# Kernel tuning notes

Hardware: AMD Instinct MI355X
Metric: run time of the kernel (lower is better)

The kernel has to match this reference:

```python
import jax, jax.numpy as jnp
import numpy as np

N, C, HID, B, K = 10000, 64, 64, 32, 2

def setup_inputs() -> dict:
    key = jax.random.key(0)
    k1, k2, k3, k4 = jax.random.split(key, 4)
    return {
        "x": jax.random.normal(k1, (B, N, C), dtype=jnp.float32),
        "node_embeddings": jax.random.normal(k2, (N, C, C), dtype=jnp.float32),
        "weights_pool": jax.random.normal(k3, (K, N, C, HID), dtype=jnp.float32),
        "bias_pool": jax.random.normal(k4, (N, HID), dtype=jnp.float32),
    }

def reference(x, node_embeddings, weights_pool, bias_pool):
    # supports: per-node adjacency-like mixing matrix, softmax(relu(.)) over last dim
    supports = jax.nn.softmax(jax.nn.relu(node_embeddings), axis=2)  # (n, c, c)
    # k=0 support is identity -> x_g[:,0] == x (no need to materialize eye)
    x_g1 = jnp.einsum('bnc,ncm->bnm', x, supports)                    # (b, n, c)
    # x_gconv = sum_k x_g[k] @ W[k] per node, + per-node bias
    out = (jnp.einsum('bnm,nmo->bno', x, weights_pool[0])
           + jnp.einsum('bnm,nmo->bno', x_g1, weights_pool[1])
           + bias_pool)                                               # (b, n, hid)
    return out
```

## Files before the change

### kernel.cpp

```cpp
#include <hip/hip_runtime.h>
#include <hip/hip_bf16.h>


constexpr int N_ = 10000;
constexpr int C_ = 64;
constexpr int H_ = 64;
constexpr int B_ = 32;
constexpr int STP = 67;

typedef __bf16 bf16x8 __attribute__((ext_vector_type(8)));
typedef float  f32x4  __attribute__((ext_vector_type(4)));

__global__ __launch_bounds__(256, 2) void avwgcn_kernel(
    const float* __restrict__ x,
    const float* __restrict__ emb,
    const float* __restrict__ wpool,
    const float* __restrict__ bias,
    float* __restrict__ out)
{
    __shared__ float st[64 * STP];
    __shared__ float g1[32 * STP];

    const int n = blockIdx.x;
    const int t = threadIdx.x;
    const int w = t >> 6;
    const int l = t & 63;
    const int r = l & 15;
    const int g = l >> 4;

    {
        const int c = t >> 2;
        const int q = t & 3;
        const float* ep = emb + (size_t)n * (C_ * C_) + c * C_ + q * 16;
        float v[16];
        #pragma unroll
        for (int i = 0; i < 4; ++i) {
            float4 e4 = *reinterpret_cast<const float4*>(ep + i * 4);
            v[i * 4 + 0] = e4.x; v[i * 4 + 1] = e4.y;
            v[i * 4 + 2] = e4.z; v[i * 4 + 3] = e4.w;
        }
        float s = 0.f;
        #pragma unroll
        for (int i = 0; i < 16; ++i) {
            float e = __expf(fmaxf(v[i], 0.f));
            v[i] = e;
            s += e;
        }
        s += __shfl_xor(s, 1);
        s += __shfl_xor(s, 2);
        const float inv = 1.0f / s;
        #pragma unroll
        for (int i = 0; i < 16; ++i)
            st[(q * 16 + i) * STP + c] = v[i] * inv;
    }

    bf16x8 xa[2][2];
    #pragma unroll
    for (int mt = 0; mt < 2; ++mt) {
        #pragma unroll
        for (int kt = 0; kt < 2; ++kt) {
            const float* xp = x + (size_t)(mt * 16 + r) * (N_ * C_)
                                + (size_t)n * C_ + kt * 32 + g * 8;
            float4 a0 = *reinterpret_cast<const float4*>(xp);
            float4 a1 = *reinterpret_cast<const float4*>(xp + 4);
            bf16x8 f;
            f[0] = (__bf16)a0.x; f[1] = (__bf16)a0.y;
            f[2] = (__bf16)a0.z; f[3] = (__bf16)a0.w;
            f[4] = (__bf16)a1.x; f[5] = (__bf16)a1.y;
            f[6] = (__bf16)a1.z; f[7] = (__bf16)a1.w;
            xa[mt][kt] = f;
        }
    }

    __syncthreads();

    f32x4 accg[2];
    accg[0] = (f32x4){0.f, 0.f, 0.f, 0.f};
    accg[1] = (f32x4){0.f, 0.f, 0.f, 0.f};
    #pragma unroll
    for (int kt = 0; kt < 2; ++kt) {
        const float* sp = st + (w * 16 + r) * STP + kt * 32 + g * 8;
        bf16x8 sb;
        #pragma unroll
        for (int i = 0; i < 8; ++i) sb[i] = (__bf16)sp[i];
        #pragma unroll
        for (int mt = 0; mt < 2; ++mt)
            accg[mt] = __builtin_amdgcn_mfma_f32_16x16x32_bf16(
                xa[mt][kt], sb, accg[mt], 0, 0, 0);
    }

    #pragma unroll
    for (int mt = 0; mt < 2; ++mt)
        #pragma unroll
        for (int ri = 0; ri < 4; ++ri)
            g1[(mt * 16 + g * 4 + ri) * STP + (w * 16 + r)] = accg[mt][ri];

    __syncthreads();

    bf16x8 ga[2][2];
    #pragma unroll
    for (int mt = 0; mt < 2; ++mt) {
        #pragma unroll
        for (int kt = 0; kt < 2; ++kt) {
            const float* gp = g1 + (mt * 16 + r) * STP + kt * 32 + g * 8;
            bf16x8 f;
            #pragma unroll
            for (int i = 0; i < 8; ++i) f[i] = (__bf16)gp[i];
            ga[mt][kt] = f;
        }
    }

    f32x4 acc[2];
    acc[0] = (f32x4){0.f, 0.f, 0.f, 0.f};
    acc[1] = (f32x4){0.f, 0.f, 0.f, 0.f};

    const float* w0 = wpool + (size_t)n * (C_ * H_);
    const float* w1 = wpool + ((size_t)N_ + n) * (C_ * H_);

    #pragma unroll
    for (int kt = 0; kt < 2; ++kt) {
        const float* wp = w0 + (size_t)(kt * 32 + g * 8) * H_ + w * 16 + r;
        bf16x8 wb;
        #pragma unroll
        for (int i = 0; i < 8; ++i) wb[i] = (__bf16)wp[i * H_];
        #pragma unroll
        for (int mt = 0; mt < 2; ++mt)
            acc[mt] = __builtin_amdgcn_mfma_f32_16x16x32_bf16(
                xa[mt][kt], wb, acc[mt], 0, 0, 0);
    }
    #pragma unroll
    for (int kt = 0; kt < 2; ++kt) {
        const float* wp = w1 + (size_t)(kt * 32 + g * 8) * H_ + w * 16 + r;
        bf16x8 wb;
        #pragma unroll
        for (int i = 0; i < 8; ++i) wb[i] = (__bf16)wp[i * H_];
        #pragma unroll
        for (int mt = 0; mt < 2; ++mt)
            acc[mt] = __builtin_amdgcn_mfma_f32_16x16x32_bf16(
                ga[mt][kt], wb, acc[mt], 0, 0, 0);
    }

    const float bv = bias[(size_t)n * H_ + w * 16 + r];
    #pragma unroll
    for (int mt = 0; mt < 2; ++mt) {
        #pragma unroll
        for (int ri = 0; ri < 4; ++ri) {
            const int b = mt * 16 + g * 4 + ri;
            const int o = w * 16 + r;
            out[(size_t)b * (N_ * H_) + (size_t)n * H_ + o] = acc[mt][ri] + bv;
        }
    }
}

extern "C" void kernel_launch(void* const* d_in, const int* in_sizes, int n_in,
                              void* d_out, int out_size, void* d_ws, size_t ws_size,
                              hipStream_t stream) {
    const float* x    = (const float*)d_in[0];
    const float* emb  = (const float*)d_in[1];
    const float* wp   = (const float*)d_in[2];
    const float* bias = (const float*)d_in[3];
    float* out = (float*)d_out;
    avwgcn_kernel<<<N_, 256, 0, stream>>>(x, emb, wp, bias, out);
}
```

Before: 143.8 us.

## Reassociate as x·(S·W1 + W0) with one node per wave

Each wave now owns a whole node, and four nodes share a block. The kernel first forms the combined matrix M = softmax(relu(E))·W1 in bf16 LDS, with the softmax normalisation folded in after the MFMA. It then computes out = x·W0 + x·M + bias, so the x·S intermediate and the block-wide __syncthreads are gone, replaced by wave-local LDS fences. Weight loads are double-buffered across the 16-column steps and occupancy is raised to 4 blocks. The matmul work per node grows (64x64x64 for M instead of 32x64x64), and rounding M to bf16 may shift accuracy.

```diff
diff --git a/kernel.cpp b/kernel.cpp
--- a/kernel.cpp
+++ b/kernel.cpp
@@ -5,151 +5,216 @@
 constexpr int N_ = 10000;
 constexpr int C_ = 64;
 constexpr int H_ = 64;
-constexpr int B_ = 32;
-constexpr int STP = 67;
+constexpr int STR = 72;
 
 typedef __bf16 bf16x8 __attribute__((ext_vector_type(8)));
 typedef float  f32x4  __attribute__((ext_vector_type(4)));
 
-__global__ __launch_bounds__(256, 2) void avwgcn_kernel(
+static __device__ __forceinline__ ushort f2b(float v) {
+    __bf16 b = (__bf16)v;
+    return __builtin_bit_cast(ushort, b);
+}
+
+static __device__ __forceinline__ void wave_lds_fence() {
+    __builtin_amdgcn_sched_barrier(0);
+    asm volatile("s_waitcnt lgkmcnt(0)" ::: "memory");
+    __builtin_amdgcn_sched_barrier(0);
+}
+
+template<int CT, bool PRE>
+static __device__ __forceinline__ void m_step(
+    const float* __restrict__ w1, ushort* st,
+    const bf16x8 (&af)[4][2], const float4 (&invc)[4],
+    float (&wcur)[2][8], float (&wnxt)[2][8], int r, int g)
+{
+    if (PRE) {
+        #pragma unroll
+        for (int kt = 0; kt < 2; ++kt)
+            #pragma unroll
+            for (int i = 0; i < 8; ++i)
+                wnxt[kt][i] = w1[(kt * 32 + g * 8 + i) * H_ + (CT + 1) * 16 + r];
+    }
+    f32x4 macc[4];
+    #pragma unroll
+    for (int rt = 0; rt < 4; ++rt) macc[rt] = (f32x4){0.f, 0.f, 0.f, 0.f};
+    #pragma unroll
+    for (int kt = 0; kt < 2; ++kt) {
+        bf16x8 wb;
+        #pragma unroll
+        for (int i = 0; i < 8; ++i) wb[i] = (__bf16)wcur[kt][i];
+        #pragma unroll
+        for (int rt = 0; rt < 4; ++rt)
+            macc[rt] = __builtin_amdgcn_mfma_f32_16x16x32_bf16(
+                af[rt][kt], wb, macc[rt], 0, 0, 0);
+    }
+    #pragma unroll
+    for (int rt = 0; rt < 4; ++rt) {
+        ushort b0 = f2b(macc[rt][0] * invc[rt].x);
+        ushort b1 = f2b(macc[rt][1] * invc[rt].y);
+        ushort b2 = f2b(macc[rt][2] * invc[rt].z);
+        ushort b3 = f2b(macc[rt][3] * invc[rt].w);
+        uint2 pk;
+        pk.x = (uint)b0 | ((uint)b1 << 16);
+        pk.y = (uint)b2 | ((uint)b3 << 16);
+        *(uint2*)(st + (CT * 16 + r) * STR + rt * 16 + g * 4) = pk;
+    }
+}
+
+template<int CT, bool PRE>
+static __device__ __forceinline__ void c_step(
+    const float* __restrict__ w0, const ushort* st,
+    const bf16x8 (&xa)[2][2], float bv,
+    float (&wcur)[2][8], float (&wnxt)[2][8],
+    float* __restrict__ outp, int r, int g)
+{
+    if (PRE) {
+        #pragma unroll
+        for (int kt = 0; kt < 2; ++kt)
+            #pragma unroll
+            for (int i = 0; i < 8; ++i)
+                wnxt[kt][i] = w0[(kt * 32 + g * 8 + i) * H_ + (CT + 1) * 16 + r];
+    }
+    bf16x8 mb[2];
+    #pragma unroll
+    for (int kt = 0; kt < 2; ++kt)
+        mb[kt] = *(const bf16x8*)(st + (CT * 16 + r) * STR + kt * 32 + g * 8);
+
+    f32x4 acc[2];
+    #pragma unroll
+    for (int mt = 0; mt < 2; ++mt) acc[mt] = (f32x4){bv, bv, bv, bv};
+
+    #pragma unroll
+    for (int kt = 0; kt < 2; ++kt) {
+        bf16x8 wb;
+        #pragma unroll
+        for (int i = 0; i < 8; ++i) wb[i] = (__bf16)wcur[kt][i];
+        #pragma unroll
+        for (int mt = 0; mt < 2; ++mt) {
+            acc[mt] = __builtin_amdgcn_mfma_f32_16x16x32_bf16(
+                xa[mt][kt], wb, acc[mt], 0, 0, 0);
+            acc[mt] = __builtin_amdgcn_mfma_f32_16x16x32_bf16(
+                xa[mt][kt], mb[kt], acc[mt], 0, 0, 0);
+        }
+    }
+    #pragma unroll
+    for (int mt = 0; mt < 2; ++mt)
+        #pragma unroll
+        for (int ri = 0; ri < 4; ++ri)
+            outp[(size_t)(mt * 16 + g * 4 + ri) * (N_ * H_) + CT * 16] = acc[mt][ri];
+}
+
+__global__ __launch_bounds__(256, 4) void avwgcn_kernel(
     const float* __restrict__ x,
     const float* __restrict__ emb,
     const float* __restrict__ wpool,
     const float* __restrict__ bias,
     float* __restrict__ out)
 {
-    __shared__ float st[64 * STP];
-    __shared__ float g1[32 * STP];
-
-    const int n = blockIdx.x;
+    __shared__ __align__(16) ushort sbuf[4][64 * STR];
+    __shared__ float inv_lds[4][64];
+
     const int t = threadIdx.x;
-    const int w = t >> 6;
+    const int wv = t >> 6;
     const int l = t & 63;
     const int r = l & 15;
     const int g = l >> 4;
+    const int n = blockIdx.x * 4 + wv;
+
+    ushort* st   = sbuf[wv];
+    float*  invp = inv_lds[wv];
 
     {
-        const int c = t >> 2;
-        const int q = t & 3;
-        const float* ep = emb + (size_t)n * (C_ * C_) + c * C_ + q * 16;
-        float v[16];
-        #pragma unroll
-        for (int i = 0; i < 4; ++i) {
-            float4 e4 = *reinterpret_cast<const float4*>(ep + i * 4);
-            v[i * 4 + 0] = e4.x; v[i * 4 + 1] = e4.y;
-            v[i * 4 + 2] = e4.z; v[i * 4 + 3] = e4.w;
+        const float* ep = emb + (size_t)n * (C_ * C_) + l * C_;
+        float sum = 0.f;
+        #pragma unroll
+        for (int c4 = 0; c4 < 4; ++c4) {
+            float4 p0 = *(const float4*)(ep + c4 * 16 + 0);
+            float4 p1 = *(const float4*)(ep + c4 * 16 + 4);
+            float4 p2 = *(const float4*)(ep + c4 * 16 + 8);
+            float4 p3 = *(const float4*)(ep + c4 * 16 + 12);
+            float v[16] = {p0.x, p0.y, p0.z, p0.w, p1.x, p1.y, p1.z, p1.w,
+                           p2.x, p2.y, p2.z, p2.w, p3.x, p3.y, p3.z, p3.w};
+            bf16x8 e0, e1;
+            #pragma unroll
+            for (int i = 0; i < 8; ++i) {
+                float a = __expf(fmaxf(v[i], 0.f));
+                float b = __expf(fmaxf(v[8 + i], 0.f));
+                sum += a + b;
+                e0[i] = (__bf16)a;
+                e1[i] = (__bf16)b;
+            }
+            *(bf16x8*)(st + l * STR + c4 * 16 + 0) = e0;
+            *(bf16x8*)(st + l * STR + c4 * 16 + 8) = e1;
         }
-        float s = 0.f;
-        #pragma unroll
-        for (int i = 0; i < 16; ++i) {
-            float e = __expf(fmaxf(v[i], 0.f));
-            v[i] = e;
-            s += e;
-        }
-        s += __shfl_xor(s, 1);
-        s += __shfl_xor(s, 2);
-        const float inv = 1.0f / s;
-        #pragma unroll
-        for (int i = 0; i < 16; ++i)
-            st[(q * 16 + i) * STP + c] = v[i] * inv;
-    }
+        invp[l] = 1.0f / sum;
+    }
+
+    wave_lds_fence();
+
+    bf16x8 af[4][2];
+    #pragma unroll
+    for (int rt = 0; rt < 4; ++rt)
+        #pragma unroll
+        for (int kt = 0; kt < 2; ++kt)
+            af[rt][kt] = *(const bf16x8*)(st + (rt * 16 + r) * STR + kt * 32 + g * 8);
+
+    float4 invc[4];
+    #pragma unroll
+    for (int rt = 0; rt < 4; ++rt)
+        invc[rt] = *(const float4*)(invp + rt * 16 + g * 4);
+
+    const float* w1 = wpool + ((size_t)N_ + n) * (C_ * H_);
+    float wlA[2][8], wlB[2][8];
+    #pragma unroll
+    for (int kt = 0; kt < 2; ++kt)
+        #pragma unroll
+        for (int i = 0; i < 8; ++i)
+            wlA[kt][i] = w1[(kt * 32 + g * 8 + i) * H_ + r];
+
+    wave_lds_fence();
+
+    m_step<0, true >(w1, st, af, invc, wlA, wlB, r, g);
+    m_step<1, true >(w1, st, af, invc, wlB, wlA, r, g);
+    m_step<2, true >(w1, st, af, invc, wlA, wlB, r, g);
+    m_step<3, false>(w1, st, af, invc, wlB, wlA, r, g);
 
     bf16x8 xa[2][2];
     #pragma unroll
-    for (int mt = 0; mt < 2; ++mt) {
+    for (int mt = 0; mt < 2; ++mt)
         #pragma unroll
         for (int kt = 0; kt < 2; ++kt) {
             const float* xp = x + (size_t)(mt * 16 + r) * (N_ * C_)
                                 + (size_t)n * C_ + kt * 32 + g * 8;
-            float4 a0 = *reinterpret_cast<const float4*>(xp);
-            float4 a1 = *reinterpret_cast<const float4*>(xp + 4);
+            float4 q0 = *(const float4*)xp;
+            float4 q1 = *(const float4*)(xp + 4);
             bf16x8 f;
-            f[0] = (__bf16)a0.x; f[1] = (__bf16)a0.y;
-            f[2] = (__bf16)a0.z; f[3] = (__bf16)a0.w;
-            f[4] = (__bf16)a1.x; f[5] = (__bf16)a1.y;
-            f[6] = (__bf16)a1.z; f[7] = (__bf16)a1.w;
+            f[0] = (__bf16)q0.x; f[1] = (__bf16)q0.y;
+            f[2] = (__bf16)q0.z; f[3] = (__bf16)q0.w;
+            f[4] = (__bf16)q1.x; f[5] = (__bf16)q1.y;
+            f[6] = (__bf16)q1.z; f[7] = (__bf16)q1.w;
             xa[mt][kt] = f;
         }
-    }
-
-    __syncthreads();
-
-    f32x4 accg[2];
-    accg[0] = (f32x4){0.f, 0.f, 0.f, 0.f};
-    accg[1] = (f32x4){0.f, 0.f, 0.f, 0.f};
-    #pragma unroll
-    for (int kt = 0; kt < 2; ++kt) {
-        const float* sp = st + (w * 16 + r) * STP + kt * 32 + g * 8;
-        bf16x8 sb;
-        #pragma unroll
-        for (int i = 0; i < 8; ++i) sb[i] = (__bf16)sp[i];
-        #pragma unroll
-        for (int mt = 0; mt < 2; ++mt)
-            accg[mt] = __builtin_amdgcn_mfma_f32_16x16x32_bf16(
-                xa[mt][kt], sb, accg[mt], 0, 0, 0);
-    }
-
-    #pragma unroll
-    for (int mt = 0; mt < 2; ++mt)
-        #pragma unroll
-        for (int ri = 0; ri < 4; ++ri)
-            g1[(mt * 16 + g * 4 + ri) * STP + (w * 16 + r)] = accg[mt][ri];
-
-    __syncthreads();
-
-    bf16x8 ga[2][2];
-    #pragma unroll
-    for (int mt = 0; mt < 2; ++mt) {
-        #pragma unroll
-        for (int kt = 0; kt < 2; ++kt) {
-            const float* gp = g1 + (mt * 16 + r) * STP + kt * 32 + g * 8;
-            bf16x8 f;
-            #pragma unroll
-            for (int i = 0; i < 8; ++i) f[i] = (__bf16)gp[i];
-            ga[mt][kt] = f;
-        }
-    }
-
-    f32x4 acc[2];
-    acc[0] = (f32x4){0.f, 0.f, 0.f, 0.f};
-    acc[1] = (f32x4){0.f, 0.f, 0.f, 0.f};
 
     const float* w0 = wpool + (size_t)n * (C_ * H_);
-    const float* w1 = wpool + ((size_t)N_ + n) * (C_ * H_);
-
-    #pragma unroll
-    for (int kt = 0; kt < 2; ++kt) {
-        const float* wp = w0 + (size_t)(kt * 32 + g * 8) * H_ + w * 16 + r;
-        bf16x8 wb;
-        #pragma unroll
-        for (int i = 0; i < 8; ++i) wb[i] = (__bf16)wp[i * H_];
-        #pragma unroll
-        for (int mt = 0; mt < 2; ++mt)
-            acc[mt] = __builtin_amdgcn_mfma_f32_16x16x32_bf16(
-                xa[mt][kt], wb, acc[mt], 0, 0, 0);
-    }
-    #pragma unroll
-    for (int kt = 0; kt < 2; ++kt) {
-        const float* wp = w1 + (size_t)(kt * 32 + g * 8) * H_ + w * 16 + r;
-        bf16x8 wb;
-        #pragma unroll
-        for (int i = 0; i < 8; ++i) wb[i] = (__bf16)wp[i * H_];
-        #pragma unroll
-        for (int mt = 0; mt < 2; ++mt)
-            acc[mt] = __builtin_amdgcn_mfma_f32_16x16x32_bf16(
-                ga[mt][kt], wb, acc[mt], 0, 0, 0);
-    }
-
-    const float bv = bias[(size_t)n * H_ + w * 16 + r];
-    #pragma unroll
-    for (int mt = 0; mt < 2; ++mt) {
-        #pragma unroll
-        for (int ri = 0; ri < 4; ++ri) {
-            const int b = mt * 16 + g * 4 + ri;
-            const int o = w * 16 + r;
-            out[(size_t)b * (N_ * H_) + (size_t)n * H_ + o] = acc[mt][ri] + bv;
-        }
-    }
+    float w0A[2][8], w0B[2][8];
+    #pragma unroll
+    for (int kt = 0; kt < 2; ++kt)
+        #pragma unroll
+        for (int i = 0; i < 8; ++i)
+            w0A[kt][i] = w0[(kt * 32 + g * 8 + i) * H_ + r];
+
+    float bv[4];
+    #pragma unroll
+    for (int ct = 0; ct < 4; ++ct)
+        bv[ct] = bias[(size_t)n * H_ + ct * 16 + r];
+
+    wave_lds_fence();
+
+    float* outp = out + (size_t)n * H_ + r;
+    c_step<0, true >(w0, st, xa, bv[0], w0A, w0B, outp, r, g);
+    c_step<1, true >(w0, st, xa, bv[1], w0B, w0A, outp, r, g);
+    c_step<2, true >(w0, st, xa, bv[2], w0A, w0B, outp, r, g);
+    c_step<3, false>(w0, st, xa, bv[3], w0B, w0A, outp, r, g);
 }
 
 extern "C" void kernel_launch(void* const* d_in, const int* in_sizes, int n_in,
@@ -160,5 +225,5 @@
     const float* wp   = (const float*)d_in[2];
     const float* bias = (const float*)d_in[3];
     float* out = (float*)d_out;
-    avwgcn_kernel<<<N_, 256, 0, stream>>>(x, emb, wp, bias, out);
-}
+    avwgcn_kernel<<<N_ / 4, 256, 0, stream>>>(x, emb, wp, bias, out);
+}
```

Result: slower. 147.9 us (+2.9%).

## Process node strips per block with double-buffered async weight loads into LDS

Applied to the files above, without the earlier changes.

Each block now handles a strip of 5 nodes instead of one. It prefetches the next node's embeddings, x and bias into registers and its weight matrices into LDS through global_load_lds, so the copies overlap the current node's compute. Intermediates are stored in LDS as bf16, and bias is folded into the accumulator init. This targets memory latency in a bandwidth-bound kernel, at the cost of 64KB of LDS per block, which lowers occupancy, and relies on a hand-tuned vmcnt count that is fragile.

```diff
diff --git a/kernel.cpp b/kernel.cpp
--- a/kernel.cpp
+++ b/kernel.cpp
@@ -1,15 +1,24 @@
 #include <hip/hip_runtime.h>
 #include <hip/hip_bf16.h>
+#include <stdint.h>
 
 
 constexpr int N_ = 10000;
 constexpr int C_ = 64;
 constexpr int H_ = 64;
-constexpr int B_ = 32;
-constexpr int STP = 67;
+constexpr int STRIP = 5;
+constexpr int GRID = N_ / STRIP;
+constexpr int STB = 72;
+
+static_assert(N_ % STRIP == 0, "strip must divide N");
 
 typedef __bf16 bf16x8 __attribute__((ext_vector_type(8)));
 typedef float  f32x4  __attribute__((ext_vector_type(4)));
+
+static __device__ __forceinline__ unsigned short f2bu(float v) {
+    __bf16 b = (__bf16)v;
+    return __builtin_bit_cast(unsigned short, b);
+}
 
 __global__ __launch_bounds__(256, 2) void avwgcn_kernel(
     const float* __restrict__ x,
@@ -18,137 +27,167 @@
     const float* __restrict__ bias,
     float* __restrict__ out)
 {
-    __shared__ float st[64 * STP];
-    __shared__ float g1[32 * STP];
-
-    const int n = blockIdx.x;
+    __shared__ float          wlds[2][2][C_ * H_];
+    __shared__ unsigned short stb[C_ * STB];
+    __shared__ unsigned short g1b[32 * STB];
+
     const int t = threadIdx.x;
-    const int w = t >> 6;
-    const int l = t & 63;
-    const int r = l & 15;
-    const int g = l >> 4;
-
-    {
-        const int c = t >> 2;
-        const int q = t & 3;
-        const float* ep = emb + (size_t)n * (C_ * C_) + c * C_ + q * 16;
-        float v[16];
-        #pragma unroll
-        for (int i = 0; i < 4; ++i) {
-            float4 e4 = *reinterpret_cast<const float4*>(ep + i * 4);
-            v[i * 4 + 0] = e4.x; v[i * 4 + 1] = e4.y;
-            v[i * 4 + 2] = e4.z; v[i * 4 + 3] = e4.w;
-        }
-        float s = 0.f;
-        #pragma unroll
-        for (int i = 0; i < 16; ++i) {
-            float e = __expf(fmaxf(v[i], 0.f));
-            v[i] = e;
-            s += e;
-        }
-        s += __shfl_xor(s, 1);
-        s += __shfl_xor(s, 2);
-        const float inv = 1.0f / s;
-        #pragma unroll
-        for (int i = 0; i < 16; ++i)
-            st[(q * 16 + i) * STP + c] = v[i] * inv;
-    }
-
-    bf16x8 xa[2][2];
+    const int w = t >> 6, l = t & 63, r = l & 15, g = l >> 4;
+    const int c = t >> 2, q = t & 3;
+    const int n0 = blockIdx.x * STRIP;
+
+    float4 ef[4];
+    float4 xf[8];
+    float  bvv[2];
+
+    auto issue = [&](int n, int buf, float& bslot) {
+        const float* ep = emb + (size_t)n * (C_ * C_) + t * 16;
+        #pragma unroll
+        for (int i = 0; i < 4; ++i) ef[i] = *(const float4*)(ep + i * 4);
+        #pragma unroll
+        for (int mt = 0; mt < 2; ++mt)
+            #pragma unroll
+            for (int kt = 0; kt < 2; ++kt) {
+                const float* xp = x + (size_t)(mt * 16 + r) * (N_ * C_)
+                                    + (size_t)n * C_ + kt * 32 + g * 8;
+                xf[mt * 4 + kt * 2 + 0] = *(const float4*)xp;
+                xf[mt * 4 + kt * 2 + 1] = *(const float4*)(xp + 4);
+            }
+        bslot = bias[(size_t)n * H_ + w * 16 + r];
+        const float* w0g = wpool + (size_t)n * (C_ * H_);
+        const float* w1g = w0g + (size_t)N_ * (C_ * H_);
+        #pragma unroll
+        for (int j = 0; j < 4; ++j) {
+            const int ch = w * 4 + j;
+            __builtin_amdgcn_global_load_lds(
+                (const __attribute__((address_space(1))) void*)(w0g + ch * 256 + l * 4),
+                (__attribute__((address_space(3))) void*)(&wlds[buf][0][ch * 256]),
+                16, 0, 0);
+        }
+        #pragma unroll
+        for (int j = 0; j < 4; ++j) {
+            const int ch = w * 4 + j;
+            __builtin_amdgcn_global_load_lds(
+                (const __attribute__((address_space(1))) void*)(w1g + ch * 256 + l * 4),
+                (__attribute__((address_space(3))) void*)(&wlds[buf][1][ch * 256]),
+                16, 0, 0);
+        }
+    };
+
+    issue(n0, 0, bvv[0]);
+
     #pragma unroll
-    for (int mt = 0; mt < 2; ++mt) {
+    for (int it = 0; it < STRIP; ++it) {
+        const int p = it & 1;
+        const int n = n0 + it;
+
+        {
+            float v[16];
+            #pragma unroll
+            for (int i = 0; i < 4; ++i) {
+                v[i*4+0] = ef[i].x; v[i*4+1] = ef[i].y;
+                v[i*4+2] = ef[i].z; v[i*4+3] = ef[i].w;
+            }
+            float s = 0.f;
+            #pragma unroll
+            for (int i = 0; i < 16; ++i) {
+                float e = __expf(fmaxf(v[i], 0.f));
+                v[i] = e; s += e;
+            }
+            s += __shfl_xor(s, 1);
+            s += __shfl_xor(s, 2);
+            const float inv = 1.0f / s;
+            #pragma unroll
+            for (int i = 0; i < 16; ++i)
+                stb[(q * 16 + i) * STB + c] = f2bu(v[i] * inv);
+        }
+        bf16x8 xa[2][2];
+        #pragma unroll
+        for (int mt = 0; mt < 2; ++mt)
+            #pragma unroll
+            for (int kt = 0; kt < 2; ++kt) {
+                float4 a0 = xf[mt * 4 + kt * 2 + 0];
+                float4 a1 = xf[mt * 4 + kt * 2 + 1];
+                bf16x8 f;
+                f[0] = (__bf16)a0.x; f[1] = (__bf16)a0.y;
+                f[2] = (__bf16)a0.z; f[3] = (__bf16)a0.w;
+                f[4] = (__bf16)a1.x; f[5] = (__bf16)a1.y;
+                f[6] = (__bf16)a1.z; f[7] = (__bf16)a1.w;
+                xa[mt][kt] = f;
+            }
+
+        __builtin_amdgcn_sched_barrier(0);
+        asm volatile("s_waitcnt lgkmcnt(0)" ::: "memory");
+        __builtin_amdgcn_s_barrier();
+        __builtin_amdgcn_sched_barrier(0);
+
+        if (it + 1 < STRIP) issue(n0 + it + 1, p ^ 1, bvv[p ^ 1]);
+
+        f32x4 accg[2];
+        accg[0] = (f32x4){0.f, 0.f, 0.f, 0.f};
+        accg[1] = (f32x4){0.f, 0.f, 0.f, 0.f};
         #pragma unroll
         for (int kt = 0; kt < 2; ++kt) {
-            const float* xp = x + (size_t)(mt * 16 + r) * (N_ * C_)
-                                + (size_t)n * C_ + kt * 32 + g * 8;
-            float4 a0 = *reinterpret_cast<const float4*>(xp);
-            float4 a1 = *reinterpret_cast<const float4*>(xp + 4);
-            bf16x8 f;
-            f[0] = (__bf16)a0.x; f[1] = (__bf16)a0.y;
-            f[2] = (__bf16)a0.z; f[3] = (__bf16)a0.w;
-            f[4] = (__bf16)a1.x; f[5] = (__bf16)a1.y;
-            f[6] = (__bf16)a1.z; f[7] = (__bf16)a1.w;
-            xa[mt][kt] = f;
-        }
-    }
-
-    __syncthreads();
-
-    f32x4 accg[2];
-    accg[0] = (f32x4){0.f, 0.f, 0.f, 0.f};
-    accg[1] = (f32x4){0.f, 0.f, 0.f, 0.f};
-    #pragma unroll
-    for (int kt = 0; kt < 2; ++kt) {
-        const float* sp = st + (w * 16 + r) * STP + kt * 32 + g * 8;
-        bf16x8 sb;
-        #pragma unroll
-        for (int i = 0; i < 8; ++i) sb[i] = (__bf16)sp[i];
-        #pragma unroll
-        for (int mt = 0; mt < 2; ++mt)
-            accg[mt] = __builtin_amdgcn_mfma_f32_16x16x32_bf16(
-                xa[mt][kt], sb, accg[mt], 0, 0, 0);
-    }
-
-    #pragma unroll
-    for (int mt = 0; mt < 2; ++mt)
-        #pragma unroll
-        for (int ri = 0; ri < 4; ++ri)
-            g1[(mt * 16 + g * 4 + ri) * STP + (w * 16 + r)] = accg[mt][ri];
-
-    __syncthreads();
-
-    bf16x8 ga[2][2];
-    #pragma unroll
-    for (int mt = 0; mt < 2; ++mt) {
+            bf16x8 sb = *(const bf16x8*)(stb + (w * 16 + r) * STB + kt * 32 + g * 8);
+            #pragma unroll
+            for (int mt = 0; mt < 2; ++mt)
+                accg[mt] = __builtin_amdgcn_mfma_f32_16x16x32_bf16(
+                    xa[mt][kt], sb, accg[mt], 0, 0, 0);
+        }
+        #pragma unroll
+        for (int mt = 0; mt < 2; ++mt)
+            #pragma unroll
+            for (int ri = 0; ri < 4; ++ri)
+                g1b[(mt * 16 + g * 4 + ri) * STB + (w * 16 + r)] = f2bu(accg[mt][ri]);
+
+        __builtin_amdgcn_sched_barrier(0);
+        if (it + 1 < STRIP)
+            asm volatile("s_waitcnt vmcnt(21) lgkmcnt(0)" ::: "memory");
+        else
+            asm volatile("s_waitcnt vmcnt(0) lgkmcnt(0)" ::: "memory");
+        __builtin_amdgcn_s_barrier();
+        __builtin_amdgcn_sched_barrier(0);
+
+        bf16x8 ga[2][2];
+        #pragma unroll
+        for (int mt = 0; mt < 2; ++mt)
+            #pragma unroll
+            for (int kt = 0; kt < 2; ++kt)
+                ga[mt][kt] = *(const bf16x8*)(g1b + (mt * 16 + r) * STB + kt * 32 + g * 8);
+
+        const float bv = bvv[p];
+        f32x4 acc[2];
+        acc[0] = (f32x4){bv, bv, bv, bv};
+        acc[1] = (f32x4){bv, bv, bv, bv};
+
+        const float* w0l = &wlds[p][0][0];
+        const float* w1l = &wlds[p][1][0];
         #pragma unroll
         for (int kt = 0; kt < 2; ++kt) {
-            const float* gp = g1 + (mt * 16 + r) * STP + kt * 32 + g * 8;
-            bf16x8 f;
-            #pragma unroll
-            for (int i = 0; i < 8; ++i) f[i] = (__bf16)gp[i];
-            ga[mt][kt] = f;
-        }
-    }
-
-    f32x4 acc[2];
-    acc[0] = (f32x4){0.f, 0.f, 0.f, 0.f};
-    acc[1] = (f32x4){0.f, 0.f, 0.f, 0.f};
-
-    const float* w0 = wpool + (size_t)n * (C_ * H_);
-    const float* w1 = wpool + ((size_t)N_ + n) * (C_ * H_);
-
-    #pragma unroll
-    for (int kt = 0; kt < 2; ++kt) {
-        const float* wp = w0 + (size_t)(kt * 32 + g * 8) * H_ + w * 16 + r;
-        bf16x8 wb;
-        #pragma unroll
-        for (int i = 0; i < 8; ++i) wb[i] = (__bf16)wp[i * H_];
-        #pragma unroll
-        for (int mt = 0; mt < 2; ++mt)
-            acc[mt] = __builtin_amdgcn_mfma_f32_16x16x32_bf16(
-                xa[mt][kt], wb, acc[mt], 0, 0, 0);
-    }
-    #pragma unroll
-    for (int kt = 0; kt < 2; ++kt) {
-        const float* wp = w1 + (size_t)(kt * 32 + g * 8) * H_ + w * 16 + r;
-        bf16x8 wb;
-        #pragma unroll
-        for (int i = 0; i < 8; ++i) wb[i] = (__bf16)wp[i * H_];
-        #pragma unroll
-        for (int mt = 0; mt < 2; ++mt)
-            acc[mt] = __builtin_amdgcn_mfma_f32_16x16x32_bf16(
-                ga[mt][kt], wb, acc[mt], 0, 0, 0);
-    }
-
-    const float bv = bias[(size_t)n * H_ + w * 16 + r];
-    #pragma unroll
-    for (int mt = 0; mt < 2; ++mt) {
-        #pragma unroll
-        for (int ri = 0; ri < 4; ++ri) {
-            const int b = mt * 16 + g * 4 + ri;
-            const int o = w * 16 + r;
-            out[(size_t)b * (N_ * H_) + (size_t)n * H_ + o] = acc[mt][ri] + bv;
-        }
+            bf16x8 wb0, wb1;
+            #pragma unroll
+            for (int i = 0; i < 8; ++i) {
+                const int idx = (kt * 32 + g * 8 + i) * H_ + w * 16 + r;
+                wb0[i] = (__bf16)w0l[idx];
+                wb1[i] = (__bf16)w1l[idx];
+            }
+            #pragma unroll
+            for (int mt = 0; mt < 2; ++mt) {
+                acc[mt] = __builtin_amdgcn_mfma_f32_16x16x32_bf16(
+                    xa[mt][kt], wb0, acc[mt], 0, 0, 0);
+                acc[mt] = __builtin_amdgcn_mfma_f32_16x16x32_bf16(
+                    ga[mt][kt], wb1, acc[mt], 0, 0, 0);
+            }
+        }
+
+        #pragma unroll
+        for (int mt = 0; mt < 2; ++mt)
+            #pragma unroll
+            for (int ri = 0; ri < 4; ++ri) {
+                const int b = mt * 16 + g * 4 + ri;
+                const int o = w * 16 + r;
+                out[(size_t)b * (N_ * H_) + (size_t)n * H_ + o] = acc[mt][ri];
+            }
     }
 }
 
@@ -160,5 +199,5 @@
     const float* wp   = (const float*)d_in[2];
     const float* bias = (const float*)d_in[3];
     float* out = (float*)d_out;
-    avwgcn_kernel<<<N_, 256, 0, stream>>>(x, emb, wp, bias, out);
+    avwgcn_kernel<<<GRID, 256, 0, stream>>>(x, emb, wp, bias, out);
 }
```

Result: no change. 142.6 us (-0.8%).
